# Kernel optimization log

Measured on AMD Instinct MI355X. Metric: run time of the kernel, lower is better.

## Reference

```python
import jax, jax.numpy as jnp
import numpy as np

EPS = 1e-06

def _feature_map(x):
    # elu(x) + 1, positive feature map
    return jax.nn.elu(x) + 1.0

def setup_inputs() -> dict:
    key = jax.random.key(0)
    k1, k2, k3 = jax.random.split(key, 3)
    B, L, d_k, d_v = 2, 4096, 128, 128
    Q = jax.random.normal(k1, (B, L, d_k), dtype=jnp.float32)
    K = jax.random.normal(k2, (B, L, d_k), dtype=jnp.float32)
    V = jax.random.normal(k3, (B, L, d_v), dtype=jnp.float32)
    return {"Q": Q, "K": K, "V": V}

def reference(Q, K, V):
    # Causal linear attention (ELU feature map).
    # out_l = phi(Q_l) @ sum_{j<=l} phi(K_j)^T V_j
    # Z_l   = phi(Q_l) . sum_{j<=l} phi(K_j)
    phiQ = _feature_map(Q)                       # (B, L, dk)
    phiK = _feature_map(K)                       # (B, L, dk)
    # cumulative KV state: (B, L, dk, dv) -- parallel replacement of the
    # original per-step bmm loop
    KV = jnp.cumsum(phiK[..., :, None] * V[..., None, :], axis=1)
    out = jnp.einsum('blk,blkv->blv', phiQ, KV)  # (B, L, dv)
    Kc = jnp.cumsum(phiK, axis=1)                # (B, L, dk)
    Z = jnp.einsum('blk,blk->bl', phiQ, Kc)[..., None]  # (B, L, 1)
    return out / (Z + EPS)
```

## Files before the change

### kernel.cpp

```cpp
#include <hip/hip_runtime.h>


#define EPS 1e-6f

constexpr int Bc = 2;
constexpr int L  = 4096;
constexpr int D  = 128;
constexpr int C  = 128;
constexpr int NC = L / C;
constexpr int P  = 136;

typedef short sh8 __attribute__((ext_vector_type(8)));
typedef float f4  __attribute__((ext_vector_type(4)));

__device__ __forceinline__ float phi(float x) {
    return x > 0.0f ? x + 1.0f : __expf(x);
}
__device__ __forceinline__ unsigned short f2bf(float f) {
    unsigned u = __float_as_uint(f);
    return (unsigned short)((u + 0x7FFFu + ((u >> 16) & 1u)) >> 16);
}
__device__ __forceinline__ float bf2f(unsigned short h) {
    return __uint_as_float(((unsigned)h) << 16);
}
__device__ __forceinline__ sh8 splat1() {
    sh8 s;
#pragma unroll
    for (int j = 0; j < 8; ++j) s[j] = (short)0x3F80;
    return s;
}

__global__ __launch_bounds__(512) void k1(
    const float* __restrict__ K, const float* __restrict__ V,
    unsigned short* __restrict__ SB, float* __restrict__ Ksum,
    unsigned short* __restrict__ KB, unsigned short* __restrict__ VT) {
    const int c = blockIdx.x, b = blockIdx.y, vs = blockIdx.z;
    const int tid = threadIdx.x;
    __shared__ __align__(16) unsigned short sVT[64 * P];
    __shared__ __align__(16) unsigned short sKT[128 * P];
    const size_t base = ((size_t)b * L + (size_t)c * C) * D;

    for (int k = 0; k < 4; ++k) {
        int fi = tid + 512 * k;
        int l = fi >> 4, c4 = fi & 15;
        float4 vd = *(const float4*)(V + base + (size_t)l * D + vs * 64 + c4 * 4);
        int blk = (((l >> 3) + c4) & 15) * 8 + (l & 7);
        sVT[(c4 * 4 + 0) * P + blk] = f2bf(vd.x);
        sVT[(c4 * 4 + 1) * P + blk] = f2bf(vd.y);
        sVT[(c4 * 4 + 2) * P + blk] = f2bf(vd.z);
        sVT[(c4 * 4 + 3) * P + blk] = f2bf(vd.w);
    }
    for (int k = 0; k < 8; ++k) {
        int fi = tid + 512 * k;
        int l = fi >> 5, i4 = fi & 31;
        float4 kd = *(const float4*)(K + base + (size_t)l * D + i4 * 4);
        int blk = (((l >> 3) + i4) & 15) * 8 + (l & 7);
        unsigned short h0 = f2bf(phi(kd.x)), h1 = f2bf(phi(kd.y));
        unsigned short h2 = f2bf(phi(kd.z)), h3 = f2bf(phi(kd.w));
        sKT[(i4 * 4 + 0) * P + blk] = h0;
        sKT[(i4 * 4 + 1) * P + blk] = h1;
        sKT[(i4 * 4 + 2) * P + blk] = h2;
        sKT[(i4 * 4 + 3) * P + blk] = h3;
        if (vs == 0) {
            uint2 pk;
            pk.x = (unsigned)h0 | ((unsigned)h1 << 16);
            pk.y = (unsigned)h2 | ((unsigned)h3 << 16);
            *(uint2*)(KB + base + (size_t)l * D + i4 * 4) = pk;
        }
    }
    __syncthreads();

    {
        const size_t vtb = (size_t)(b * NC + c) * D * 128 + (size_t)vs * 64 * 128;
        for (int k = 0; k < 2; ++k) {
            int idx = tid + 512 * k;
            int vr = idx >> 4, c8 = idx & 15;
            *(uint4*)(VT + vtb + vr * 128 + c8 * 8) =
                *(const uint4*)(sVT + vr * P + c8 * 8);
        }
    }

    const int w = tid >> 6, lane = tid & 63;
    const int r = lane & 15, q = lane >> 4;
    const int rbase = (w & 3) * 16;
    const int cbase = (w >> 2) * 64;
    const bool doK = ((w & 3) == 0);
    const sh8 ones = splat1();

    f4 acc[4], kz[4];
#pragma unroll
    for (int f = 0; f < 4; ++f) { acc[f] = {0.f,0.f,0.f,0.f}; kz[f] = {0.f,0.f,0.f,0.f}; }
#pragma unroll
    for (int ks = 0; ks < 4; ++ks) {
        int kq = ks * 4 + q;
        int vr = rbase + r;
        sh8 a = *(const sh8*)(sVT + vr * P + ((kq + (vr >> 2)) & 15) * 8);
#pragma unroll
        for (int f = 0; f < 4; ++f) {
            int ir = cbase + f * 16 + r;
            sh8 bk = *(const sh8*)(sKT + ir * P + ((kq + (ir >> 2)) & 15) * 8);
            acc[f] = __builtin_amdgcn_mfma_f32_16x16x32_bf16(a, bk, acc[f], 0, 0, 0);
            if (doK) kz[f] = __builtin_amdgcn_mfma_f32_16x16x32_bf16(ones, bk, kz[f], 0, 0, 0);
        }
    }
    unsigned short* out = SB + ((size_t)(b * NC + c)) * D * D;
#pragma unroll
    for (int f = 0; f < 4; ++f) {
        int i = cbase + f * 16 + r;
#pragma unroll
        for (int e = 0; e < 4; ++e) {
            int v = vs * 64 + rbase + q * 4 + e;
            out[(size_t)v * D + i] = f2bf(acc[f][e]);
        }
    }
    if (doK && q == 0 && vs == 0) {
#pragma unroll
        for (int f = 0; f < 4; ++f)
            Ksum[((size_t)(b * NC + c)) * D + cbase + f * 16 + r] = kz[f][0];
    }
}

__global__ __launch_bounds__(256) void k_scan(unsigned short* __restrict__ SB,
                                              float* __restrict__ Ksum) {
    const int SD = D * D;
    int idx = blockIdx.x * 256 + threadIdx.x;
    if (idx < Bc * SD) {
        int b = idx / SD, e = idx % SD;
        size_t off0 = (size_t)b * NC * SD + e;
        unsigned short vals[NC];
#pragma unroll
        for (int c = 0; c < NC; ++c) vals[c] = SB[off0 + (size_t)c * SD];
        float run = 0.0f;
#pragma unroll
        for (int c = 0; c < NC; ++c) {
            SB[off0 + (size_t)c * SD] = f2bf(run);
            run += bf2f(vals[c]);
        }
    } else if (idx < Bc * SD + Bc * D) {
        int rr = idx - Bc * SD;
        int b = rr >> 7, i = rr & 127;
        size_t off0 = (size_t)b * NC * D + i;
        float vals[NC];
#pragma unroll
        for (int c = 0; c < NC; ++c) vals[c] = Ksum[off0 + (size_t)c * D];
        float run = 0.0f;
#pragma unroll
        for (int c = 0; c < NC; ++c) {
            Ksum[off0 + (size_t)c * D] = run;
            run += vals[c];
        }
    }
}

__global__ __launch_bounds__(512) void k_out(
    const float* __restrict__ Q, const unsigned short* __restrict__ KB,
    const unsigned short* __restrict__ VT, const unsigned short* __restrict__ SB,
    const float* __restrict__ Ksum, float* __restrict__ Out) {
    const int c = blockIdx.x, b = blockIdx.y, rs = blockIdx.z;
    const int tid = threadIdx.x;
    __shared__ __align__(16) unsigned short sK[128 * P];
    __shared__ __align__(16) unsigned short sVT[128 * P];
    __shared__ __align__(16) unsigned short sAm[32 * P];
    __shared__ float sZ[32];
    const size_t obase = ((size_t)b * L + (size_t)c * C) * D;
    const size_t tbase = (size_t)(b * NC + c) * (size_t)D * D;
    const size_t vtb   = (size_t)(b * NC + c) * (size_t)D * 128;
    const size_t kb    = (size_t)(b * NC + c) * D;

    for (int k = 0; k < 4; ++k) {
        int fi = tid + 512 * k;
        int row = fi >> 4, c8 = fi & 15;
        *(uint4*)(sK + row * P + c8 * 8) =
            *(const uint4*)(KB + obase + (size_t)row * D + c8 * 8);
    }
    for (int k = 0; k < 4; ++k) {
        int fi = tid + 512 * k;
        int vr = fi >> 4, c8 = fi & 15;
        *(uint4*)(sVT + vr * P + c8 * 8) =
            *(const uint4*)(VT + vtb + (size_t)vr * 128 + c8 * 8);
    }

    const int w = tid >> 6, lane = tid & 63;
    const int r = lane & 15, q = lane >> 4;
    const int rbase = (w & 1) * 16;
    const int cq = w >> 1, cbase = cq * 32;
    const bool doZ = (cq == 3);

    sh8 qf[4];
    {
        const float* qrow = Q + obase + (size_t)(rs * 32 + rbase + r) * D;
#pragma unroll
        for (int ks = 0; ks < 4; ++ks) {
            float4 a0 = *(const float4*)(qrow + ks * 32 + q * 8);
            float4 a1 = *(const float4*)(qrow + ks * 32 + q * 8 + 4);
            sh8 t;
            t[0] = (short)f2bf(phi(a0.x)); t[1] = (short)f2bf(phi(a0.y));
            t[2] = (short)f2bf(phi(a0.z)); t[3] = (short)f2bf(phi(a0.w));
            t[4] = (short)f2bf(phi(a1.x)); t[5] = (short)f2bf(phi(a1.y));
            t[6] = (short)f2bf(phi(a1.z)); t[7] = (short)f2bf(phi(a1.w));
            qf[ks] = t;
        }
    }

    sh8 bzk[4];
    if (doZ) {
#pragma unroll
        for (int ks = 0; ks < 4; ++ks) {
            float4 f0 = *(const float4*)(Ksum + kb + ks * 32 + q * 8);
            float4 f1 = *(const float4*)(Ksum + kb + ks * 32 + q * 8 + 4);
            sh8 t;
            t[0] = (short)f2bf(f0.x); t[1] = (short)f2bf(f0.y);
            t[2] = (short)f2bf(f0.z); t[3] = (short)f2bf(f0.w);
            t[4] = (short)f2bf(f1.x); t[5] = (short)f2bf(f1.y);
            t[6] = (short)f2bf(f1.z); t[7] = (short)f2bf(f1.w);
            bzk[ks] = t;
        }
    }
    __syncthreads();

    f4 a2[2];
#pragma unroll
    for (int f = 0; f < 2; ++f) a2[f] = {0.f,0.f,0.f,0.f};
#pragma unroll
    for (int ks = 0; ks < 4; ++ks) {
#pragma unroll
        for (int f = 0; f < 2; ++f) {
            sh8 bb = *(const sh8*)(sK + (cbase + f * 16 + r) * P + ks * 32 + q * 8);
            a2[f] = __builtin_amdgcn_mfma_f32_16x16x32_bf16(qf[ks], bb, a2[f], 0, 0, 0);
        }
    }
#pragma unroll
    for (int f = 0; f < 2; ++f) {
        int j = cbase + f * 16 + r;
#pragma unroll
        for (int e = 0; e < 4; ++e) {
            int lr = rbase + q * 4 + e;
            sAm[lr * P + j] = f2bf((j <= rs * 32 + lr) ? a2[f][e] : 0.f);
        }
    }
    __syncthreads();

    {
        const uint4* sg = (const uint4*)(SB + tbase);
        for (int k = 0; k < 4; ++k) {
            int f2 = tid + 512 * k;
            *(uint4*)(sK + (f2 >> 4) * P + (f2 & 15) * 8) = sg[f2];
        }
    }

    f4 acc[2], zacc = {0.f,0.f,0.f,0.f};
#pragma unroll
    for (int f = 0; f < 2; ++f) acc[f] = {0.f,0.f,0.f,0.f};
    const sh8 ones = splat1();
#pragma unroll
    for (int ks = 0; ks < 4; ++ks) {
        int kq = ks * 4 + q;
        sh8 a = *(const sh8*)(sAm + (rbase + r) * P + ks * 32 + q * 8);
#pragma unroll
        for (int f = 0; f < 2; ++f) {
            int vr = cbase + f * 16 + r;
            sh8 bv = *(const sh8*)(sVT + vr * P + ((kq + (vr >> 2)) & 15) * 8);
            acc[f] = __builtin_amdgcn_mfma_f32_16x16x32_bf16(a, bv, acc[f], 0, 0, 0);
        }
        if (doZ) zacc = __builtin_amdgcn_mfma_f32_16x16x32_bf16(a, ones, zacc, 0, 0, 0);
    }
    __syncthreads();

#pragma unroll
    for (int ks = 0; ks < 4; ++ks) {
#pragma unroll
        for (int f = 0; f < 2; ++f) {
            sh8 bs = *(const sh8*)(sK + (cbase + f * 16 + r) * P + ks * 32 + q * 8);
            acc[f] = __builtin_amdgcn_mfma_f32_16x16x32_bf16(qf[ks], bs, acc[f], 0, 0, 0);
        }
        if (doZ) zacc = __builtin_amdgcn_mfma_f32_16x16x32_bf16(qf[ks], bzk[ks], zacc, 0, 0, 0);
    }
    if (doZ && r == 0) {
#pragma unroll
        for (int e = 0; e < 4; ++e) sZ[rbase + q * 4 + e] = zacc[e] + EPS;
    }
    __syncthreads();

#pragma unroll
    for (int f = 0; f < 2; ++f) {
        int v = cbase + f * 16 + r;
#pragma unroll
        for (int e = 0; e < 4; ++e) {
            int lr = rbase + q * 4 + e;
            Out[obase + (size_t)(rs * 32 + lr) * D + v] = acc[f][e] / sZ[lr];
        }
    }
}

extern "C" void kernel_launch(void* const* d_in, const int* in_sizes, int n_in,
                              void* d_out, int out_size, void* d_ws, size_t ws_size,
                              hipStream_t stream) {
    const float* Q = (const float*)d_in[0];
    const float* K = (const float*)d_in[1];
    const float* V = (const float*)d_in[2];
    float* Out = (float*)d_out;
    const size_t SB_BYTES = (size_t)Bc * NC * D * D * 2;
    unsigned short* SBw = (unsigned short*)d_ws;
    unsigned short* KBw = (unsigned short*)((char*)d_ws + SB_BYTES);
    unsigned short* VTw = (unsigned short*)((char*)d_ws + 2 * SB_BYTES);
    float* Ksum = (float*)((char*)d_ws + 3 * SB_BYTES);

    k1<<<dim3(NC, Bc, 2), 512, 0, stream>>>(K, V, SBw, Ksum, KBw, VTw);
    int total = Bc * D * D + Bc * D;
    k_scan<<<dim3((total + 255) / 256), 256, 0, stream>>>(SBw, Ksum);
    k_out<<<dim3(NC, Bc, 4), 512, 0, stream>>>(Q, KBw, VTw, SBw, Ksum, Out);
}
```

Before: 80.17 us.

## Split k1 over key halves, vectorize chunk scan, prefetch prefix state early

k1 now splits the 128-wide key dimension across two more grid blocks, doubling the block count from 128 to 256 and halving per-block shared memory and K loads. The scan kernel handles eight bf16 state elements (and four Ksum floats) per thread with 128-bit loads and stores, which cuts thread count and memory transactions. k_out issues the global loads of the prefix state into registers before the first matmul phase so their latency overlaps compute. The trade-offs are that V is reloaded by both key halves, the scan launches fewer threads (less parallelism), and k_out uses more registers.

```diff
diff --git a/kernel.cpp b/kernel.cpp
--- a/kernel.cpp
+++ b/kernel.cpp
@@ -23,6 +23,9 @@
 __device__ __forceinline__ float bf2f(unsigned short h) {
     return __uint_as_float(((unsigned)h) << 16);
 }
+__device__ __forceinline__ unsigned packbf(float a, float b) {
+    return (unsigned)f2bf(a) | ((unsigned)f2bf(b) << 16);
+}
 __device__ __forceinline__ sh8 splat1() {
     sh8 s;
 #pragma unroll
@@ -34,10 +37,11 @@
     const float* __restrict__ K, const float* __restrict__ V,
     unsigned short* __restrict__ SB, float* __restrict__ Ksum,
     unsigned short* __restrict__ KB, unsigned short* __restrict__ VT) {
-    const int c = blockIdx.x, b = blockIdx.y, vs = blockIdx.z;
+    const int c = blockIdx.x, b = blockIdx.y;
+    const int vs = blockIdx.z & 1, is = blockIdx.z >> 1;
     const int tid = threadIdx.x;
     __shared__ __align__(16) unsigned short sVT[64 * P];
-    __shared__ __align__(16) unsigned short sKT[128 * P];
+    __shared__ __align__(16) unsigned short sKT[64 * P];
     const size_t base = ((size_t)b * L + (size_t)c * C) * D;
 
     for (int k = 0; k < 4; ++k) {
@@ -50,10 +54,10 @@
         sVT[(c4 * 4 + 2) * P + blk] = f2bf(vd.z);
         sVT[(c4 * 4 + 3) * P + blk] = f2bf(vd.w);
     }
-    for (int k = 0; k < 8; ++k) {
+    for (int k = 0; k < 4; ++k) {
         int fi = tid + 512 * k;
-        int l = fi >> 5, i4 = fi & 31;
-        float4 kd = *(const float4*)(K + base + (size_t)l * D + i4 * 4);
+        int l = fi >> 4, i4 = fi & 15;
+        float4 kd = *(const float4*)(K + base + (size_t)l * D + is * 64 + i4 * 4);
         int blk = (((l >> 3) + i4) & 15) * 8 + (l & 7);
         unsigned short h0 = f2bf(phi(kd.x)), h1 = f2bf(phi(kd.y));
         unsigned short h2 = f2bf(phi(kd.z)), h3 = f2bf(phi(kd.w));
@@ -65,12 +69,12 @@
             uint2 pk;
             pk.x = (unsigned)h0 | ((unsigned)h1 << 16);
             pk.y = (unsigned)h2 | ((unsigned)h3 << 16);
-            *(uint2*)(KB + base + (size_t)l * D + i4 * 4) = pk;
-        }
-    }
-    __syncthreads();
-
-    {
+            *(uint2*)(KB + base + (size_t)l * D + is * 64 + i4 * 4) = pk;
+        }
+    }
+    __syncthreads();
+
+    if (is == 0) {
         const size_t vtb = (size_t)(b * NC + c) * D * 128 + (size_t)vs * 64 * 128;
         for (int k = 0; k < 2; ++k) {
             int idx = tid + 512 * k;
@@ -83,20 +87,20 @@
     const int w = tid >> 6, lane = tid & 63;
     const int r = lane & 15, q = lane >> 4;
     const int rbase = (w & 3) * 16;
-    const int cbase = (w >> 2) * 64;
-    const bool doK = ((w & 3) == 0);
+    const int cbase = (w >> 2) * 32;
+    const bool doK = ((w & 3) == 0) && (vs == 0);
     const sh8 ones = splat1();
 
-    f4 acc[4], kz[4];
-#pragma unroll
-    for (int f = 0; f < 4; ++f) { acc[f] = {0.f,0.f,0.f,0.f}; kz[f] = {0.f,0.f,0.f,0.f}; }
+    f4 acc[2], kz[2];
+#pragma unroll
+    for (int f = 0; f < 2; ++f) { acc[f] = {0.f,0.f,0.f,0.f}; kz[f] = {0.f,0.f,0.f,0.f}; }
 #pragma unroll
     for (int ks = 0; ks < 4; ++ks) {
         int kq = ks * 4 + q;
         int vr = rbase + r;
         sh8 a = *(const sh8*)(sVT + vr * P + ((kq + (vr >> 2)) & 15) * 8);
 #pragma unroll
-        for (int f = 0; f < 4; ++f) {
+        for (int f = 0; f < 2; ++f) {
             int ir = cbase + f * 16 + r;
             sh8 bk = *(const sh8*)(sKT + ir * P + ((kq + (ir >> 2)) & 15) * 8);
             acc[f] = __builtin_amdgcn_mfma_f32_16x16x32_bf16(a, bk, acc[f], 0, 0, 0);
@@ -105,49 +109,67 @@
     }
     unsigned short* out = SB + ((size_t)(b * NC + c)) * D * D;
 #pragma unroll
-    for (int f = 0; f < 4; ++f) {
-        int i = cbase + f * 16 + r;
+    for (int f = 0; f < 2; ++f) {
+        int i = is * 64 + cbase + f * 16 + r;
 #pragma unroll
         for (int e = 0; e < 4; ++e) {
             int v = vs * 64 + rbase + q * 4 + e;
             out[(size_t)v * D + i] = f2bf(acc[f][e]);
         }
     }
-    if (doK && q == 0 && vs == 0) {
-#pragma unroll
-        for (int f = 0; f < 4; ++f)
-            Ksum[((size_t)(b * NC + c)) * D + cbase + f * 16 + r] = kz[f][0];
+    if (doK && q == 0) {
+#pragma unroll
+        for (int f = 0; f < 2; ++f)
+            Ksum[((size_t)(b * NC + c)) * D + is * 64 + cbase + f * 16 + r] = kz[f][0];
     }
 }
 
 __global__ __launch_bounds__(256) void k_scan(unsigned short* __restrict__ SB,
                                               float* __restrict__ Ksum) {
     const int SD = D * D;
+    const int nSB = Bc * SD / 8;
     int idx = blockIdx.x * 256 + threadIdx.x;
-    if (idx < Bc * SD) {
-        int b = idx / SD, e = idx % SD;
-        size_t off0 = (size_t)b * NC * SD + e;
-        unsigned short vals[NC];
-#pragma unroll
-        for (int c = 0; c < NC; ++c) vals[c] = SB[off0 + (size_t)c * SD];
-        float run = 0.0f;
+    if (idx < nSB) {
+        int b = idx / (SD / 8), e8 = idx % (SD / 8);
+        size_t off0 = (size_t)b * NC * SD + (size_t)e8 * 8;
+        uint4 vals[NC];
+#pragma unroll
+        for (int c = 0; c < NC; ++c)
+            vals[c] = *(const uint4*)(SB + off0 + (size_t)c * SD);
+        float run[8];
+#pragma unroll
+        for (int j = 0; j < 8; ++j) run[j] = 0.0f;
 #pragma unroll
         for (int c = 0; c < NC; ++c) {
-            SB[off0 + (size_t)c * SD] = f2bf(run);
-            run += bf2f(vals[c]);
-        }
-    } else if (idx < Bc * SD + Bc * D) {
-        int rr = idx - Bc * SD;
-        int b = rr >> 7, i = rr & 127;
-        size_t off0 = (size_t)b * NC * D + i;
-        float vals[NC];
-#pragma unroll
-        for (int c = 0; c < NC; ++c) vals[c] = Ksum[off0 + (size_t)c * D];
-        float run = 0.0f;
+            uint4 w;
+            w.x = packbf(run[0], run[1]);
+            w.y = packbf(run[2], run[3]);
+            w.z = packbf(run[4], run[5]);
+            w.w = packbf(run[6], run[7]);
+            *(uint4*)(SB + off0 + (size_t)c * SD) = w;
+            run[0] += bf2f((unsigned short)(vals[c].x & 0xFFFF));
+            run[1] += bf2f((unsigned short)(vals[c].x >> 16));
+            run[2] += bf2f((unsigned short)(vals[c].y & 0xFFFF));
+            run[3] += bf2f((unsigned short)(vals[c].y >> 16));
+            run[4] += bf2f((unsigned short)(vals[c].z & 0xFFFF));
+            run[5] += bf2f((unsigned short)(vals[c].z >> 16));
+            run[6] += bf2f((unsigned short)(vals[c].w & 0xFFFF));
+            run[7] += bf2f((unsigned short)(vals[c].w >> 16));
+        }
+    } else if (idx < nSB + Bc * D / 4) {
+        int rr = idx - nSB;
+        int b = rr >> 5, i4 = rr & 31;
+        size_t off0 = (size_t)b * NC * D + (size_t)i4 * 4;
+        float4 vals[NC];
+#pragma unroll
+        for (int c = 0; c < NC; ++c)
+            vals[c] = *(const float4*)(Ksum + off0 + (size_t)c * D);
+        float4 run = {0.f, 0.f, 0.f, 0.f};
 #pragma unroll
         for (int c = 0; c < NC; ++c) {
-            Ksum[off0 + (size_t)c * D] = run;
-            run += vals[c];
+            *(float4*)(Ksum + off0 + (size_t)c * D) = run;
+            run.x += vals[c].x; run.y += vals[c].y;
+            run.z += vals[c].z; run.w += vals[c].w;
         }
     }
 }
@@ -180,6 +202,13 @@
             *(const uint4*)(VT + vtb + (size_t)vr * 128 + c8 * 8);
     }
 
+    uint4 sbv[4];
+    {
+        const uint4* sg = (const uint4*)(SB + tbase);
+#pragma unroll
+        for (int k = 0; k < 4; ++k) sbv[k] = sg[tid + 512 * k];
+    }
+
     const int w = tid >> 6, lane = tid & 63;
     const int r = lane & 15, q = lane >> 4;
     const int rbase = (w & 1) * 16;
@@ -240,12 +269,10 @@
     }
     __syncthreads();
 
-    {
-        const uint4* sg = (const uint4*)(SB + tbase);
-        for (int k = 0; k < 4; ++k) {
-            int f2 = tid + 512 * k;
-            *(uint4*)(sK + (f2 >> 4) * P + (f2 & 15) * 8) = sg[f2];
-        }
+#pragma unroll
+    for (int k = 0; k < 4; ++k) {
+        int f2 = tid + 512 * k;
+        *(uint4*)(sK + (f2 >> 4) * P + (f2 & 15) * 8) = sbv[k];
     }
 
     f4 acc[2], zacc = {0.f,0.f,0.f,0.f};
@@ -305,8 +332,8 @@
     unsigned short* VTw = (unsigned short*)((char*)d_ws + 2 * SB_BYTES);
     float* Ksum = (float*)((char*)d_ws + 3 * SB_BYTES);
 
-    k1<<<dim3(NC, Bc, 2), 512, 0, stream>>>(K, V, SBw, Ksum, KBw, VTw);
-    int total = Bc * D * D + Bc * D;
-    k_scan<<<dim3((total + 255) / 256), 256, 0, stream>>>(SBw, Ksum);
+    k1<<<dim3(NC, Bc, 4), 512, 0, stream>>>(K, V, SBw, Ksum, KBw, VTw);
+    int totalThreads = Bc * D * D / 8 + Bc * D / 4;
+    k_scan<<<dim3((totalThreads + 255) / 256), 256, 0, stream>>>(SBw, Ksum);
     k_out<<<dim3(NC, Bc, 4), 512, 0, stream>>>(Q, KBw, VTw, SBw, Ksum, Out);
 }
```

New measurement: 82.62 us. +3.1%, slower.

## Fold cross-chunk prefix scan into output kernel, removing separate scan launch

Applied to the files above, without the earlier changes.

Removes the k_scan kernel that computed exclusive prefix sums over per-chunk KV states and key sums. Each k_out block now sums all preceding chunk states itself in fp32 registers before packing them to bf16 in shared memory. This saves a kernel launch and the scan's global read-write pass. In exchange it adds redundant reads that grow with the chunk index (quadratic total traffic, with 4 z-slices repeating the work) and load imbalance across blocks.

```diff
diff --git a/kernel.cpp b/kernel.cpp
--- a/kernel.cpp
+++ b/kernel.cpp
@@ -20,8 +20,14 @@
     unsigned u = __float_as_uint(f);
     return (unsigned short)((u + 0x7FFFu + ((u >> 16) & 1u)) >> 16);
 }
-__device__ __forceinline__ float bf2f(unsigned short h) {
-    return __uint_as_float(((unsigned)h) << 16);
+__device__ __forceinline__ float bflo(unsigned u) {
+    return __uint_as_float(u << 16);
+}
+__device__ __forceinline__ float bfhi(unsigned u) {
+    return __uint_as_float(u & 0xFFFF0000u);
+}
+__device__ __forceinline__ unsigned packbf(float a, float b) {
+    return (unsigned)f2bf(a) | ((unsigned)f2bf(b) << 16);
 }
 __device__ __forceinline__ sh8 splat1() {
     sh8 s;
@@ -120,38 +126,6 @@
     }
 }
 
-__global__ __launch_bounds__(256) void k_scan(unsigned short* __restrict__ SB,
-                                              float* __restrict__ Ksum) {
-    const int SD = D * D;
-    int idx = blockIdx.x * 256 + threadIdx.x;
-    if (idx < Bc * SD) {
-        int b = idx / SD, e = idx % SD;
-        size_t off0 = (size_t)b * NC * SD + e;
-        unsigned short vals[NC];
-#pragma unroll
-        for (int c = 0; c < NC; ++c) vals[c] = SB[off0 + (size_t)c * SD];
-        float run = 0.0f;
-#pragma unroll
-        for (int c = 0; c < NC; ++c) {
-            SB[off0 + (size_t)c * SD] = f2bf(run);
-            run += bf2f(vals[c]);
-        }
-    } else if (idx < Bc * SD + Bc * D) {
-        int rr = idx - Bc * SD;
-        int b = rr >> 7, i = rr & 127;
-        size_t off0 = (size_t)b * NC * D + i;
-        float vals[NC];
-#pragma unroll
-        for (int c = 0; c < NC; ++c) vals[c] = Ksum[off0 + (size_t)c * D];
-        float run = 0.0f;
-#pragma unroll
-        for (int c = 0; c < NC; ++c) {
-            Ksum[off0 + (size_t)c * D] = run;
-            run += vals[c];
-        }
-    }
-}
-
 __global__ __launch_bounds__(512) void k_out(
     const float* __restrict__ Q, const unsigned short* __restrict__ KB,
     const unsigned short* __restrict__ VT, const unsigned short* __restrict__ SB,
@@ -163,9 +137,8 @@
     __shared__ __align__(16) unsigned short sAm[32 * P];
     __shared__ float sZ[32];
     const size_t obase = ((size_t)b * L + (size_t)c * C) * D;
-    const size_t tbase = (size_t)(b * NC + c) * (size_t)D * D;
     const size_t vtb   = (size_t)(b * NC + c) * (size_t)D * 128;
-    const size_t kb    = (size_t)(b * NC + c) * D;
+    const int SD = D * D;
 
     for (int k = 0; k < 4; ++k) {
         int fi = tid + 512 * k;
@@ -202,17 +175,44 @@
         }
     }
 
+    float sacc[32];
+#pragma unroll
+    for (int j = 0; j < 32; ++j) sacc[j] = 0.f;
+#pragma unroll 2
+    for (int cp = 0; cp < c; ++cp) {
+        const uint4* sg = (const uint4*)(SB + (size_t)(b * NC + cp) * SD);
+#pragma unroll
+        for (int k = 0; k < 4; ++k) {
+            uint4 vv = sg[tid + 512 * k];
+            sacc[k * 8 + 0] += bflo(vv.x); sacc[k * 8 + 1] += bfhi(vv.x);
+            sacc[k * 8 + 2] += bflo(vv.y); sacc[k * 8 + 3] += bfhi(vv.y);
+            sacc[k * 8 + 4] += bflo(vv.z); sacc[k * 8 + 5] += bfhi(vv.z);
+            sacc[k * 8 + 6] += bflo(vv.w); sacc[k * 8 + 7] += bfhi(vv.w);
+        }
+    }
+
     sh8 bzk[4];
     if (doZ) {
+        float kzacc[32];
+#pragma unroll
+        for (int j = 0; j < 32; ++j) kzacc[j] = 0.f;
+        for (int cp = 0; cp < c; ++cp) {
+            const float* kp = Ksum + (size_t)(b * NC + cp) * D;
+#pragma unroll
+            for (int ks = 0; ks < 4; ++ks) {
+                float4 f0 = *(const float4*)(kp + ks * 32 + q * 8);
+                float4 f1 = *(const float4*)(kp + ks * 32 + q * 8 + 4);
+                kzacc[ks * 8 + 0] += f0.x; kzacc[ks * 8 + 1] += f0.y;
+                kzacc[ks * 8 + 2] += f0.z; kzacc[ks * 8 + 3] += f0.w;
+                kzacc[ks * 8 + 4] += f1.x; kzacc[ks * 8 + 5] += f1.y;
+                kzacc[ks * 8 + 6] += f1.z; kzacc[ks * 8 + 7] += f1.w;
+            }
+        }
 #pragma unroll
         for (int ks = 0; ks < 4; ++ks) {
-            float4 f0 = *(const float4*)(Ksum + kb + ks * 32 + q * 8);
-            float4 f1 = *(const float4*)(Ksum + kb + ks * 32 + q * 8 + 4);
             sh8 t;
-            t[0] = (short)f2bf(f0.x); t[1] = (short)f2bf(f0.y);
-            t[2] = (short)f2bf(f0.z); t[3] = (short)f2bf(f0.w);
-            t[4] = (short)f2bf(f1.x); t[5] = (short)f2bf(f1.y);
-            t[6] = (short)f2bf(f1.z); t[7] = (short)f2bf(f1.w);
+#pragma unroll
+            for (int j = 0; j < 8; ++j) t[j] = (short)f2bf(kzacc[ks * 8 + j]);
             bzk[ks] = t;
         }
     }
@@ -240,12 +240,15 @@
     }
     __syncthreads();
 
-    {
-        const uint4* sg = (const uint4*)(SB + tbase);
-        for (int k = 0; k < 4; ++k) {
-            int f2 = tid + 512 * k;
-            *(uint4*)(sK + (f2 >> 4) * P + (f2 & 15) * 8) = sg[f2];
-        }
+#pragma unroll
+    for (int k = 0; k < 4; ++k) {
+        int f2 = tid + 512 * k;
+        uint4 wv;
+        wv.x = packbf(sacc[k * 8 + 0], sacc[k * 8 + 1]);
+        wv.y = packbf(sacc[k * 8 + 2], sacc[k * 8 + 3]);
+        wv.z = packbf(sacc[k * 8 + 4], sacc[k * 8 + 5]);
+        wv.w = packbf(sacc[k * 8 + 6], sacc[k * 8 + 7]);
+        *(uint4*)(sK + (f2 >> 4) * P + (f2 & 15) * 8) = wv;
     }
 
     f4 acc[2], zacc = {0.f,0.f,0.f,0.f};
@@ -306,7 +309,5 @@
     float* Ksum = (float*)((char*)d_ws + 3 * SB_BYTES);
 
     k1<<<dim3(NC, Bc, 2), 512, 0, stream>>>(K, V, SBw, Ksum, KBw, VTw);
-    int total = Bc * D * D + Bc * D;
-    k_scan<<<dim3((total + 255) / 256), 256, 0, stream>>>(SBw, Ksum);
     k_out<<<dim3(NC, Bc, 4), 512, 0, stream>>>(Q, KBw, VTw, SBw, Ksum, Out);
 }
```

Measured after the change: 109.4 us. 36.5% more time.
